# Kernel optimization log

Measured on AMD Instinct MI355X. Metric: run time of the kernel, lower is better.

## Reference

```python
import jax, jax.numpy as jnp
import numpy as np

EPS = 1e-5

def _layer_norm(x, gamma, beta):
    mu = jnp.mean(x, axis=-1, keepdims=True)
    var = jnp.var(x, axis=-1, keepdims=True)
    return (x - mu) * jax.lax.rsqrt(var + EPS) * gamma + beta

def setup_inputs() -> dict:
    key = jax.random.key(0)
    ks = jax.random.split(key, 4)
    B, T, D, H = 16, 2048, 1024, 1024
    s_in = 1.0 / np.sqrt(D)
    return {
        "x": jax.random.normal(ks[0], (B, T, D), dtype=jnp.float32),
        "c": jnp.zeros((B, H), dtype=jnp.float32),
        "W_lt": jax.random.uniform(ks[1], (H, D), jnp.float32, -s_in, s_in),
        "W_g": jax.random.uniform(ks[2], (2 * H, D), jnp.float32, -s_in, s_in),
        "b_g": jnp.zeros((2 * H,), dtype=jnp.float32),
        "gamma_g": jnp.ones((2 * H,), dtype=jnp.float32),
        "beta_g": jnp.zeros((2 * H,), dtype=jnp.float32),
        "gamma_a": jnp.ones((H,), dtype=jnp.float32),
        "beta_a": jnp.zeros((H,), dtype=jnp.float32),
    }

def reference(x, c, W_lt, W_g, b_g, gamma_g, beta_g, gamma_a, beta_a):
    H = W_lt.shape[0]
    # x: [B,T,D]
    x_tilde = jnp.einsum("btd,hd->bth", x, W_lt)            # [B,T,H]
    gate = jax.nn.sigmoid(_layer_norm(jnp.einsum("btd,gd->btg", x, W_g) + b_g, gamma_g, beta_g))
    f = gate[:, :, :H]                                        # forget gate [B,T,H]
    r = gate[:, :, H:]                                        # reset gate  [B,T,H]
    new_data = (1.0 - f) * x_tilde

    def step(c_prev, ft_nd):
        f_t, nd_t = ft_nd
        c_t = f_t * c_prev + nd_t
        return c_t, c_t

    # scan over time: move T to leading axis
    c_final, all_c = jax.lax.scan(step, c, (jnp.swapaxes(f, 0, 1), jnp.swapaxes(new_data, 0, 1)))
    all_c = jnp.swapaxes(all_c, 0, 1)                         # [B,T,H]
    h = r * jax.nn.sigmoid(_layer_norm(all_c, gamma_a, beta_a)) + (1.0 - r) * x
    return (h, c_final)
```

## Files before the change

kernel.cpp:

```cpp
#include <hip/hip_runtime.h>
#include <stdint.h>

typedef unsigned short u16;
typedef u16 us8 __attribute__((ext_vector_type(8)));
typedef __bf16 bf16x8 __attribute__((ext_vector_type(8)));
typedef float f32x4 __attribute__((ext_vector_type(4)));

#define BB 16
#define TT 2048
#define HH 1024
#define MM 32768
#define NN 3072
#define KK 1024

__device__ __forceinline__ float b2f(u16 u) {
    union { uint32_t i; float f; } v; v.i = ((uint32_t)u) << 16; return v.f;
}
__device__ __forceinline__ u16 f2b(float f) {
    union { uint32_t i; float f; } v; v.f = f;
    uint32_t r = v.i + 0x7fffu + ((v.i >> 16) & 1u);
    return (u16)(r >> 16);
}
__device__ __forceinline__ float sigm(float z) {
    return 1.f / (1.f + __expf(-z));
}

__global__ __launch_bounds__(256) void k_cvt_x(const float* __restrict__ x,
                                               u16* __restrict__ o) {
    int i = (blockIdx.x * 256 + threadIdx.x) * 8;
    float4 a = *(const float4*)(x + i);
    float4 b = *(const float4*)(x + i + 4);
    us8 r;
    r[0] = f2b(a.x); r[1] = f2b(a.y); r[2] = f2b(a.z); r[3] = f2b(a.w);
    r[4] = f2b(b.x); r[5] = f2b(b.y); r[6] = f2b(b.z); r[7] = f2b(b.w);
    *(us8*)(o + i) = r;
}

__global__ __launch_bounds__(256) void k_cvt_w(const float* __restrict__ wlt,
                                               const float* __restrict__ wg,
                                               u16* __restrict__ o) {
    int i = (blockIdx.x * 256 + threadIdx.x) * 8;
    const float* s = (i < 1024 * 1024) ? (wlt + i) : (wg + (i - 1024 * 1024));
    float4 a = *(const float4*)(s);
    float4 b = *(const float4*)(s + 4);
    us8 r;
    r[0] = f2b(a.x); r[1] = f2b(a.y); r[2] = f2b(a.z); r[3] = f2b(a.w);
    r[4] = f2b(b.x); r[5] = f2b(b.y); r[6] = f2b(b.z); r[7] = f2b(b.w);
    *(us8*)(o + i) = r;
}

__global__ __launch_bounds__(256) void k_gemm(const u16* __restrict__ A,
                                              const u16* __restrict__ W,
                                              u16* __restrict__ Y) {
    __shared__ u16 As[128 * 32];
    __shared__ u16 Bs[128 * 32];
    const int tid = threadIdx.x;
    const int lane = tid & 63;
    const int q = lane >> 4;
    const int l16 = lane & 15;
    const int w = tid >> 6;
    const int wm = (w >> 1) * 64, wn = (w & 1) * 64;
    const int bx = blockIdx.x, by = blockIdx.y;

    const int s0 = tid, s1 = tid + 256;
    const int r0 = s0 >> 2, c0 = (s0 & 3) * 8;
    const int r1 = s1 >> 2, c1 = (s1 & 3) * 8;
    const u16* a0 = A + (by * 128 + r0) * KK + c0;
    const u16* a1 = A + (by * 128 + r1) * KK + c1;
    const u16* w0 = W + (bx * 128 + r0) * KK + c0;
    const u16* w1 = W + (bx * 128 + r1) * KK + c1;
    const int d0 = r0 * 4 + ((s0 & 3) ^ (r0 & 3));
    const int d1 = r1 * 4 + ((s1 & 3) ^ (r1 & 3));

    f32x4 zero = {0.f, 0.f, 0.f, 0.f};
    f32x4 acc[4][4];
#pragma unroll
    for (int i = 0; i < 4; i++)
#pragma unroll
        for (int j = 0; j < 4; j++) acc[i][j] = zero;

    for (int k0 = 0; k0 < KK; k0 += 32) {
        uint4 va0 = *(const uint4*)(a0 + k0);
        uint4 va1 = *(const uint4*)(a1 + k0);
        uint4 vb0 = *(const uint4*)(w0 + k0);
        uint4 vb1 = *(const uint4*)(w1 + k0);
        __syncthreads();
        ((uint4*)As)[d0] = va0;
        ((uint4*)As)[d1] = va1;
        ((uint4*)Bs)[d0] = vb0;
        ((uint4*)Bs)[d1] = vb1;
        __syncthreads();
        bf16x8 af[4], bv[4];
#pragma unroll
        for (int i = 0; i < 4; i++) {
            int r = wm + i * 16 + l16;
            af[i] = *(const bf16x8*)&As[(r * 4 + (q ^ (r & 3))) * 8];
        }
#pragma unroll
        for (int j = 0; j < 4; j++) {
            int r = wn + j * 16 + l16;
            bv[j] = *(const bf16x8*)&Bs[(r * 4 + (q ^ (r & 3))) * 8];
        }
#pragma unroll
        for (int i = 0; i < 4; i++)
#pragma unroll
            for (int j = 0; j < 4; j++)
                acc[i][j] = __builtin_amdgcn_mfma_f32_16x16x32_bf16(
                    af[i], bv[j], acc[i][j], 0, 0, 0);
    }

#pragma unroll
    for (int i = 0; i < 4; i++) {
#pragma unroll
        for (int rg = 0; rg < 4; rg++) {
            int row = by * 128 + wm + i * 16 + q * 4 + rg;
            u16* yp = Y + (size_t)row * NN + bx * 128 + wn + l16;
#pragma unroll
            for (int j = 0; j < 4; j++) yp[j * 16] = f2b(acc[i][j][rg]);
        }
    }
}

__global__ __launch_bounds__(256) void k_lnsig(const u16* __restrict__ Y,
                                               const float* __restrict__ bg,
                                               const float* __restrict__ gg,
                                               const float* __restrict__ bt,
                                               u16* __restrict__ F,
                                               u16* __restrict__ R,
                                               u16* __restrict__ ND) {
    const int row = blockIdx.x;
    const int t = threadIdx.x;
    const u16* yr = Y + (size_t)row * 3072;
    us8 gv = *(const us8*)(yr + 1024 + t * 8);
    float z[8];
    float s = 0.f, s2 = 0.f;
#pragma unroll
    for (int k = 0; k < 8; k++) {
        z[k] = b2f(gv[k]) + bg[t * 8 + k];
        s += z[k];
        s2 += z[k] * z[k];
    }
#pragma unroll
    for (int m = 1; m < 64; m <<= 1) {
        s += __shfl_xor(s, m);
        s2 += __shfl_xor(s2, m);
    }
    __shared__ float red[8];
    if ((t & 63) == 0) { red[t >> 6] = s; red[(t >> 6) + 4] = s2; }
    __syncthreads();
    s = red[0] + red[1] + red[2] + red[3];
    s2 = red[4] + red[5] + red[6] + red[7];
    const float mu = s * (1.f / 2048.f);
    const float inv = rsqrtf(s2 * (1.f / 2048.f) - mu * mu + 1e-5f);
    float gate[8];
#pragma unroll
    for (int k = 0; k < 8; k++)
        gate[k] = sigm((z[k] - mu) * inv * gg[t * 8 + k] + bt[t * 8 + k]);
    if (t < 128) {
        us8 xt = *(const us8*)(yr + t * 8);
        us8 fo, no;
#pragma unroll
        for (int k = 0; k < 8; k++) {
            fo[k] = f2b(gate[k]);
            no[k] = f2b((1.f - gate[k]) * b2f(xt[k]));
        }
        *(us8*)(F + (size_t)row * 1024 + t * 8) = fo;
        *(us8*)(ND + (size_t)row * 1024 + t * 8) = no;
    } else {
        us8 ro;
#pragma unroll
        for (int k = 0; k < 8; k++) ro[k] = f2b(gate[k]);
        *(us8*)(R + (size_t)row * 1024 + (t - 128) * 8) = ro;
    }
}

__global__ __launch_bounds__(256) void k_scan1(const u16* __restrict__ F,
                                               const u16* __restrict__ ND,
                                               float2* __restrict__ agg) {
    int u = blockIdx.x * 256 + threadIdx.x;
    int h = u & 1023;
    int chunk = (u >> 10) & 31;
    int b = u >> 15;
    int base = (b * 2048 + chunk * 64) * 1024 + h;
    float Fp = 1.f, Np = 0.f;
#pragma unroll 4
    for (int i = 0; i < 64; i++) {
        float f = b2f(F[base + i * 1024]);
        float n = b2f(ND[base + i * 1024]);
        Np = fmaf(f, Np, n);
        Fp *= f;
    }
    agg[(b * 1024 + h) * 32 + chunk] = make_float2(Fp, Np);
}

__global__ __launch_bounds__(256) void k_scan2(const float2* __restrict__ agg,
                                               const float* __restrict__ c0,
                                               float* __restrict__ P) {
    int u = blockIdx.x * 256 + threadIdx.x;
    float c = c0[u];
    const float2* a = agg + (size_t)u * 32;
    float* p = P + (size_t)u * 32;
#pragma unroll 4
    for (int k = 0; k < 32; k++) {
        p[k] = c;
        float2 fn = a[k];
        c = fmaf(fn.x, c, fn.y);
    }
}

__global__ __launch_bounds__(256) void k_scan3(const u16* __restrict__ F,
                                               const u16* __restrict__ ND,
                                               const float* __restrict__ P,
                                               u16* __restrict__ C,
                                               float* __restrict__ cfin) {
    int u = blockIdx.x * 256 + threadIdx.x;
    int h = u & 1023;
    int chunk = (u >> 10) & 31;
    int b = u >> 15;
    int base = (b * 2048 + chunk * 64) * 1024 + h;
    float c = P[(b * 1024 + h) * 32 + chunk];
#pragma unroll 4
    for (int i = 0; i < 64; i++) {
        float f = b2f(F[base + i * 1024]);
        float n = b2f(ND[base + i * 1024]);
        c = fmaf(f, c, n);
        C[base + i * 1024] = f2b(c);
    }
    if (chunk == 31) cfin[b * 1024 + h] = c;
}

__global__ __launch_bounds__(256) void k_final(const u16* __restrict__ C,
                                               const u16* __restrict__ R,
                                               const float* __restrict__ x,
                                               const float* __restrict__ ga,
                                               const float* __restrict__ ba,
                                               float* __restrict__ Ho) {
    const int w = threadIdx.x >> 6, lane = threadIdx.x & 63;
    const int row = blockIdx.x * 4 + w;
    const int col = lane * 16;
    const u16* cp = C + (size_t)row * 1024 + col;
    us8 cv0 = *(const us8*)cp;
    us8 cv1 = *(const us8*)(cp + 8);
    float c[16];
    float s = 0.f, s2 = 0.f;
#pragma unroll
    for (int k = 0; k < 8; k++) { c[k] = b2f(cv0[k]); c[8 + k] = b2f(cv1[k]); }
#pragma unroll
    for (int k = 0; k < 16; k++) { s += c[k]; s2 += c[k] * c[k]; }
#pragma unroll
    for (int m = 1; m < 64; m <<= 1) {
        s += __shfl_xor(s, m);
        s2 += __shfl_xor(s2, m);
    }
    const float mu = s * (1.f / 1024.f);
    const float inv = rsqrtf(s2 * (1.f / 1024.f) - mu * mu + 1e-5f);
    const u16* rp = R + (size_t)row * 1024 + col;
    us8 rv0 = *(const us8*)rp;
    us8 rv1 = *(const us8*)(rp + 8);
    const float* xp = x + (size_t)row * 1024 + col;
    float xv[16];
    *(float4*)&xv[0]  = *(const float4*)(xp);
    *(float4*)&xv[4]  = *(const float4*)(xp + 4);
    *(float4*)&xv[8]  = *(const float4*)(xp + 8);
    *(float4*)&xv[12] = *(const float4*)(xp + 12);
    float ho[16];
#pragma unroll
    for (int k = 0; k < 16; k++) {
        float sg = sigm((c[k] - mu) * inv * ga[col + k] + ba[col + k]);
        float rr = b2f(k < 8 ? rv0[k] : rv1[k - 8]);
        ho[k] = rr * sg + (1.f - rr) * xv[k];
    }
    float* op = Ho + (size_t)row * 1024 + col;
    *(float4*)(op)      = *(float4*)&ho[0];
    *(float4*)(op + 4)  = *(float4*)&ho[4];
    *(float4*)(op + 8)  = *(float4*)&ho[8];
    *(float4*)(op + 12) = *(float4*)&ho[12];
}

extern "C" void kernel_launch(void* const* d_in, const int* in_sizes, int n_in,
                              void* d_out, int out_size, void* d_ws, size_t ws_size,
                              hipStream_t stream) {
    const float* x   = (const float*)d_in[0];
    const float* c0  = (const float*)d_in[1];
    const float* wlt = (const float*)d_in[2];
    const float* wg  = (const float*)d_in[3];
    const float* bg  = (const float*)d_in[4];
    const float* gg  = (const float*)d_in[5];
    const float* btg = (const float*)d_in[6];
    const float* ga  = (const float*)d_in[7];
    const float* ba  = (const float*)d_in[8];
    float* out = (float*)d_out;

    char* ws = (char*)d_ws;
    u16* xb    = (u16*)(ws);
    u16* wb    = (u16*)(ws + 67108864);
    u16* y     = (u16*)(ws + 73400320);
    u16* F     = (u16*)(ws + 274726912);
    u16* R     = (u16*)(ws + 341835776);
    u16* ND    = (u16*)(ws + 408944640);
    float2* agg = (float2*)(ws + 476053504);
    float* P   = (float*)(ws + 480247808);
    u16* C     = y;

    k_cvt_x<<<16384, 256, 0, stream>>>(x, xb);
    k_cvt_w<<<1536, 256, 0, stream>>>(wlt, wg, wb);
    k_gemm<<<dim3(24, 256), 256, 0, stream>>>(xb, wb, y);
    k_lnsig<<<32768, 256, 0, stream>>>(y, bg, gg, btg, F, R, ND);
    k_scan1<<<2048, 256, 0, stream>>>(F, ND, agg);
    k_scan2<<<64, 256, 0, stream>>>(agg, c0, P);
    k_scan3<<<2048, 256, 0, stream>>>(F, ND, P, C, out + (size_t)33554432);
    k_final<<<8192, 256, 0, stream>>>(C, R, x, ga, ba, out);
}
```

Measured before the change: 754.9 us.

## Use direct global-to-LDS loads in GEMM, interleave F/ND, read bf16 x

Merges the x and weight conversion kernels into one launch. The GEMM now stages tiles with global_load_lds instead of going through registers, and drops the XOR swizzle. The forget gate and new_data are packed into one 32-bit word per element so the scan kernels issue a single load. The final kernel reads the bf16 copy of x instead of fp32. Together these cut memory traffic and register staging, at the cost of possible LDS bank conflicts and reduced precision in the residual term.

```diff
diff --git a/kernel.cpp b/kernel.cpp
--- a/kernel.cpp
+++ b/kernel.cpp
@@ -3,6 +3,7 @@
 
 typedef unsigned short u16;
 typedef u16 us8 __attribute__((ext_vector_type(8)));
+typedef uint32_t u32x8 __attribute__((ext_vector_type(8)));
 typedef __bf16 bf16x8 __attribute__((ext_vector_type(8)));
 typedef float f32x4 __attribute__((ext_vector_type(4)));
 
@@ -24,29 +25,32 @@
 __device__ __forceinline__ float sigm(float z) {
     return 1.f / (1.f + __expf(-z));
 }
-
-__global__ __launch_bounds__(256) void k_cvt_x(const float* __restrict__ x,
-                                               u16* __restrict__ o) {
-    int i = (blockIdx.x * 256 + threadIdx.x) * 8;
-    float4 a = *(const float4*)(x + i);
-    float4 b = *(const float4*)(x + i + 4);
-    us8 r;
-    r[0] = f2b(a.x); r[1] = f2b(a.y); r[2] = f2b(a.z); r[3] = f2b(a.w);
-    r[4] = f2b(b.x); r[5] = f2b(b.y); r[6] = f2b(b.z); r[7] = f2b(b.w);
-    *(us8*)(o + i) = r;
-}
-
-__global__ __launch_bounds__(256) void k_cvt_w(const float* __restrict__ wlt,
-                                               const float* __restrict__ wg,
-                                               u16* __restrict__ o) {
-    int i = (blockIdx.x * 256 + threadIdx.x) * 8;
-    const float* s = (i < 1024 * 1024) ? (wlt + i) : (wg + (i - 1024 * 1024));
+__device__ __forceinline__ void load_lds16(const u16* g, u16* l) {
+    __builtin_amdgcn_global_load_lds(
+        (const __attribute__((address_space(1))) void*)g,
+        (__attribute__((address_space(3))) void*)l, 16, 0, 0);
+}
+
+__global__ __launch_bounds__(256) void k_cvt(const float* __restrict__ x,
+                                             const float* __restrict__ wlt,
+                                             const float* __restrict__ wg,
+                                             u16* __restrict__ xb,
+                                             u16* __restrict__ wb) {
+    long i = (long)(blockIdx.x * 256 + threadIdx.x) * 8;
+    const float* s;
+    u16* o;
+    if (i < 33554432L) { s = x + i; o = xb + i; }
+    else {
+        long j = i - 33554432L;
+        s = (j < 1048576L) ? (wlt + j) : (wg + (j - 1048576L));
+        o = wb + j;
+    }
     float4 a = *(const float4*)(s);
     float4 b = *(const float4*)(s + 4);
     us8 r;
     r[0] = f2b(a.x); r[1] = f2b(a.y); r[2] = f2b(a.z); r[3] = f2b(a.w);
     r[4] = f2b(b.x); r[5] = f2b(b.y); r[6] = f2b(b.z); r[7] = f2b(b.w);
-    *(us8*)(o + i) = r;
+    *(us8*)o = r;
 }
 
 __global__ __launch_bounds__(256) void k_gemm(const u16* __restrict__ A,
@@ -62,15 +66,16 @@
     const int wm = (w >> 1) * 64, wn = (w & 1) * 64;
     const int bx = blockIdx.x, by = blockIdx.y;
 
-    const int s0 = tid, s1 = tid + 256;
-    const int r0 = s0 >> 2, c0 = (s0 & 3) * 8;
-    const int r1 = s1 >> 2, c1 = (s1 & 3) * 8;
-    const u16* a0 = A + (by * 128 + r0) * KK + c0;
-    const u16* a1 = A + (by * 128 + r1) * KK + c1;
-    const u16* w0 = W + (bx * 128 + r0) * KK + c0;
-    const u16* w1 = W + (bx * 128 + r1) * KK + c1;
-    const int d0 = r0 * 4 + ((s0 & 3) ^ (r0 & 3));
-    const int d1 = r1 * 4 + ((s1 & 3) ^ (r1 & 3));
+    const int s0 = w * 128 + lane;
+    const int s1 = w * 128 + 64 + lane;
+    const u16* ag0 = A + (size_t)(by * 128 + (s0 >> 2)) * KK + (s0 & 3) * 8;
+    const u16* ag1 = A + (size_t)(by * 128 + (s1 >> 2)) * KK + (s1 & 3) * 8;
+    const u16* wg0 = W + (size_t)(bx * 128 + (s0 >> 2)) * KK + (s0 & 3) * 8;
+    const u16* wg1 = W + (size_t)(bx * 128 + (s1 >> 2)) * KK + (s1 & 3) * 8;
+    u16* al0 = As + w * 1024;
+    u16* al1 = As + w * 1024 + 512;
+    u16* bl0 = Bs + w * 1024;
+    u16* bl1 = Bs + w * 1024 + 512;
 
     f32x4 zero = {0.f, 0.f, 0.f, 0.f};
     f32x4 acc[4][4];
@@ -80,27 +85,19 @@
         for (int j = 0; j < 4; j++) acc[i][j] = zero;
 
     for (int k0 = 0; k0 < KK; k0 += 32) {
-        uint4 va0 = *(const uint4*)(a0 + k0);
-        uint4 va1 = *(const uint4*)(a1 + k0);
-        uint4 vb0 = *(const uint4*)(w0 + k0);
-        uint4 vb1 = *(const uint4*)(w1 + k0);
         __syncthreads();
-        ((uint4*)As)[d0] = va0;
-        ((uint4*)As)[d1] = va1;
-        ((uint4*)Bs)[d0] = vb0;
-        ((uint4*)Bs)[d1] = vb1;
+        load_lds16(ag0 + k0, al0);
+        load_lds16(ag1 + k0, al1);
+        load_lds16(wg0 + k0, bl0);
+        load_lds16(wg1 + k0, bl1);
         __syncthreads();
         bf16x8 af[4], bv[4];
 #pragma unroll
-        for (int i = 0; i < 4; i++) {
-            int r = wm + i * 16 + l16;
-            af[i] = *(const bf16x8*)&As[(r * 4 + (q ^ (r & 3))) * 8];
-        }
-#pragma unroll
-        for (int j = 0; j < 4; j++) {
-            int r = wn + j * 16 + l16;
-            bv[j] = *(const bf16x8*)&Bs[(r * 4 + (q ^ (r & 3))) * 8];
-        }
+        for (int i = 0; i < 4; i++)
+            af[i] = *(const bf16x8*)&As[(wm + i * 16 + l16) * 32 + q * 8];
+#pragma unroll
+        for (int j = 0; j < 4; j++)
+            bv[j] = *(const bf16x8*)&Bs[(wn + j * 16 + l16) * 32 + q * 8];
 #pragma unroll
         for (int i = 0; i < 4; i++)
 #pragma unroll
@@ -125,9 +122,8 @@
                                                const float* __restrict__ bg,
                                                const float* __restrict__ gg,
                                                const float* __restrict__ bt,
-                                               u16* __restrict__ F,
-                                               u16* __restrict__ R,
-                                               u16* __restrict__ ND) {
+                                               uint32_t* __restrict__ FN,
+                                               u16* __restrict__ R) {
     const int row = blockIdx.x;
     const int t = threadIdx.x;
     const u16* yr = Y + (size_t)row * 3072;
@@ -158,14 +154,14 @@
         gate[k] = sigm((z[k] - mu) * inv * gg[t * 8 + k] + bt[t * 8 + k]);
     if (t < 128) {
         us8 xt = *(const us8*)(yr + t * 8);
-        us8 fo, no;
+        u32x8 fn;
 #pragma unroll
         for (int k = 0; k < 8; k++) {
-            fo[k] = f2b(gate[k]);
-            no[k] = f2b((1.f - gate[k]) * b2f(xt[k]));
+            u16 fb = f2b(gate[k]);
+            u16 nb = f2b((1.f - gate[k]) * b2f(xt[k]));
+            fn[k] = (uint32_t)fb | ((uint32_t)nb << 16);
         }
-        *(us8*)(F + (size_t)row * 1024 + t * 8) = fo;
-        *(us8*)(ND + (size_t)row * 1024 + t * 8) = no;
+        *(u32x8*)(FN + (size_t)row * 1024 + t * 8) = fn;
     } else {
         us8 ro;
 #pragma unroll
@@ -174,8 +170,7 @@
     }
 }
 
-__global__ __launch_bounds__(256) void k_scan1(const u16* __restrict__ F,
-                                               const u16* __restrict__ ND,
+__global__ __launch_bounds__(256) void k_scan1(const uint32_t* __restrict__ FN,
                                                float2* __restrict__ agg) {
     int u = blockIdx.x * 256 + threadIdx.x;
     int h = u & 1023;
@@ -185,8 +180,9 @@
     float Fp = 1.f, Np = 0.f;
 #pragma unroll 4
     for (int i = 0; i < 64; i++) {
-        float f = b2f(F[base + i * 1024]);
-        float n = b2f(ND[base + i * 1024]);
+        uint32_t v = FN[base + i * 1024];
+        float f = b2f((u16)(v & 0xffffu));
+        float n = b2f((u16)(v >> 16));
         Np = fmaf(f, Np, n);
         Fp *= f;
     }
@@ -208,8 +204,7 @@
     }
 }
 
-__global__ __launch_bounds__(256) void k_scan3(const u16* __restrict__ F,
-                                               const u16* __restrict__ ND,
+__global__ __launch_bounds__(256) void k_scan3(const uint32_t* __restrict__ FN,
                                                const float* __restrict__ P,
                                                u16* __restrict__ C,
                                                float* __restrict__ cfin) {
@@ -221,8 +216,9 @@
     float c = P[(b * 1024 + h) * 32 + chunk];
 #pragma unroll 4
     for (int i = 0; i < 64; i++) {
-        float f = b2f(F[base + i * 1024]);
-        float n = b2f(ND[base + i * 1024]);
+        uint32_t v = FN[base + i * 1024];
+        float f = b2f((u16)(v & 0xffffu));
+        float n = b2f((u16)(v >> 16));
         c = fmaf(f, c, n);
         C[base + i * 1024] = f2b(c);
     }
@@ -231,7 +227,7 @@
 
 __global__ __launch_bounds__(256) void k_final(const u16* __restrict__ C,
                                                const u16* __restrict__ R,
-                                               const float* __restrict__ x,
+                                               const u16* __restrict__ xb,
                                                const float* __restrict__ ga,
                                                const float* __restrict__ ba,
                                                float* __restrict__ Ho) {
@@ -257,18 +253,16 @@
     const u16* rp = R + (size_t)row * 1024 + col;
     us8 rv0 = *(const us8*)rp;
     us8 rv1 = *(const us8*)(rp + 8);
-    const float* xp = x + (size_t)row * 1024 + col;
-    float xv[16];
-    *(float4*)&xv[0]  = *(const float4*)(xp);
-    *(float4*)&xv[4]  = *(const float4*)(xp + 4);
-    *(float4*)&xv[8]  = *(const float4*)(xp + 8);
-    *(float4*)&xv[12] = *(const float4*)(xp + 12);
+    const u16* xp = xb + (size_t)row * 1024 + col;
+    us8 xv0 = *(const us8*)xp;
+    us8 xv1 = *(const us8*)(xp + 8);
     float ho[16];
 #pragma unroll
     for (int k = 0; k < 16; k++) {
         float sg = sigm((c[k] - mu) * inv * ga[col + k] + ba[col + k]);
         float rr = b2f(k < 8 ? rv0[k] : rv1[k - 8]);
-        ho[k] = rr * sg + (1.f - rr) * xv[k];
+        float xx = b2f(k < 8 ? xv0[k] : xv1[k - 8]);
+        ho[k] = rr * sg + (1.f - rr) * xx;
     }
     float* op = Ho + (size_t)row * 1024 + col;
     *(float4*)(op)      = *(float4*)&ho[0];
@@ -292,22 +286,20 @@
     float* out = (float*)d_out;
 
     char* ws = (char*)d_ws;
-    u16* xb    = (u16*)(ws);
-    u16* wb    = (u16*)(ws + 67108864);
-    u16* y     = (u16*)(ws + 73400320);
-    u16* F     = (u16*)(ws + 274726912);
-    u16* R     = (u16*)(ws + 341835776);
-    u16* ND    = (u16*)(ws + 408944640);
-    float2* agg = (float2*)(ws + 476053504);
-    float* P   = (float*)(ws + 480247808);
-    u16* C     = y;
-
-    k_cvt_x<<<16384, 256, 0, stream>>>(x, xb);
-    k_cvt_w<<<1536, 256, 0, stream>>>(wlt, wg, wb);
+    u16* xb      = (u16*)(ws);
+    u16* wb      = (u16*)(ws + 67108864);
+    u16* y       = (u16*)(ws + 73400320);
+    uint32_t* FN = (uint32_t*)(ws + 274726912);
+    u16* R       = (u16*)(ws + 408944640);
+    float2* agg  = (float2*)(ws + 476053504);
+    float* P     = (float*)(ws + 480247808);
+    u16* C       = y;
+
+    k_cvt<<<17920, 256, 0, stream>>>(x, wlt, wg, xb, wb);
     k_gemm<<<dim3(24, 256), 256, 0, stream>>>(xb, wb, y);
-    k_lnsig<<<32768, 256, 0, stream>>>(y, bg, gg, btg, F, R, ND);
-    k_scan1<<<2048, 256, 0, stream>>>(F, ND, agg);
+    k_lnsig<<<32768, 256, 0, stream>>>(y, bg, gg, btg, FN, R);
+    k_scan1<<<2048, 256, 0, stream>>>(FN, agg);
     k_scan2<<<64, 256, 0, stream>>>(agg, c0, P);
-    k_scan3<<<2048, 256, 0, stream>>>(F, ND, P, C, out + (size_t)33554432);
-    k_final<<<8192, 256, 0, stream>>>(C, R, x, ga, ba, out);
-}
+    k_scan3<<<2048, 256, 0, stream>>>(FN, P, C, out + (size_t)33554432);
+    k_final<<<8192, 256, 0, stream>>>(C, R, xb, ga, ba, out);
+}
```

Measured after the change: 712.4 us. 5.6% less time.
